# Kernel tuning notes

Measured on AMD Instinct MI355X. Metric: run time of the kernel, lower is better.

The kernel has to match this reference:

```python
import jax, jax.numpy as jnp
import numpy as np

BIG_K = 13
EPS = 1e-5  # torch BatchNorm2d default


def setup_inputs() -> dict:
    key = jax.random.key(0)
    k1, k2, k3, k4 = jax.random.split(key, 4)
    B, C1, C2, H, W_ = 8, 256, 256, 64, 64
    x = jax.random.normal(k1, (B, C1, H, W_), dtype=jnp.float32)
    # scale kernel by fan-in so pre-BN activations are O(1)
    fan_in = C1 * BIG_K * BIG_K
    W = jax.random.normal(k2, (C2, C1, BIG_K, BIG_K), dtype=jnp.float32) / np.sqrt(fan_in)
    gamma = jnp.ones((C2,), dtype=jnp.float32)
    beta = jnp.zeros((C2,), dtype=jnp.float32)
    running_mean = jax.random.normal(k3, (C2,), dtype=jnp.float32) * 0.1
    running_var = jax.random.uniform(k4, (C2,), dtype=jnp.float32, minval=0.5, maxval=1.5)
    return {"x": x, "W": W, "gamma": gamma, "beta": beta,
            "running_mean": running_mean, "running_var": running_var}


def reference(x, W, gamma, beta, running_mean, running_var):
    # Fallback path of ShiftWiseConv: big-kernel conv (no bias) -> BN (inference) -> SiLU
    pad = BIG_K // 2
    y = jax.lax.conv_general_dilated(
        x, W,
        window_strides=(1, 1),
        padding=[(pad, pad), (pad, pad)],
        dimension_numbers=("NCHW", "OIHW", "NCHW"),
    )
    inv = gamma * jax.lax.rsqrt(running_var + EPS)  # [C2]
    y = y * inv[None, :, None, None] + (beta - running_mean * inv)[None, :, None, None]
    return jax.nn.silu(y)
```

## Files before the change

### kernel.cpp

```cpp
#include <hip/hip_runtime.h>
#include <stdint.h>

#define EPS 1e-5f

typedef __attribute__((ext_vector_type(8))) __bf16 bf16x8;
typedef __attribute__((ext_vector_type(16))) float f32x16;

__device__ __forceinline__ int swz4(int r) { return (r ^ (r >> 2)) & 3; }

__device__ __forceinline__ unsigned short f2bf(float f) {
  union { float f; unsigned u; } v; v.f = f;
  unsigned r = v.u + 0x7fffu + ((v.u >> 16) & 1u);
  return (unsigned short)(r >> 16);
}

__device__ __forceinline__ void glds16(const unsigned short* g, unsigned short* l) {
  __builtin_amdgcn_global_load_lds(
      (const __attribute__((address_space(1))) void*)g,
      (__attribute__((address_space(3))) void*)l, 16, 0, 0);
}
__device__ __forceinline__ void glds4(const unsigned short* g, unsigned short* l) {
  __builtin_amdgcn_global_load_lds(
      (const __attribute__((address_space(1))) void*)g,
      (__attribute__((address_space(3))) void*)l, 4, 0, 0);
}

template <int N>
__device__ __forceinline__ void vmwait() {
  asm volatile("s_waitcnt vmcnt(%0)" ::"n"(N) : "memory");
}

__global__ __launch_bounds__(256) void pack_w_kernel(
    const float* __restrict__ W, unsigned short* __restrict__ Wp) {
  const int blk = blockIdx.x;
  const int c2 = blk / 13, kh = blk - c2 * 13;
  const int c1 = threadIdx.x;
  const int c2t = c2 >> 7, m = c2 & 127;
  const int c1c = c1 >> 5, c1i = c1 & 31;
  const float* src = W + (((size_t)(c2 * 256 + c1)) * 13 + kh) * 13;
  const int rowoff = (((c1i >> 3) ^ swz4(m)) << 3) + (c1i & 7);
#pragma unroll
  for (int kw = 0; kw < 13; ++kw) {
    const int ks = (kh * 8 + c1c) * 13 + kw;
    const size_t dst = (((size_t)c2t * 1352 + ks) * 128 + m) * 32 + rowoff;
    Wp[dst] = f2bf(src[kw]);
  }
}

__global__ __launch_bounds__(256) void pack_xt_kernel(
    const float* __restrict__ x, unsigned short* __restrict__ xT) {
  const int blk = blockIdx.x;
  const int rowp = blk % 76;
  const int bc = blk / 76;
  const int c1c = bc & 7, b = bc >> 3;
  const int row = rowp - 6;
  const bool rok = (unsigned)row < 64u;
  unsigned short* dst = xT + (size_t)blk * 2560;
  const float* srcb = x + (size_t)(b * 256 + c1c * 32) * 4096 +
                      (rok ? row * 64 : 0);
#pragma unroll
  for (int e = 0; e < 10; ++e) {
    const int idx = e * 256 + threadIdx.x;
    const int colp = idx >> 5, c1i = idx & 31;
    const int ic = colp - 8;
    const float v = (rok && (unsigned)ic < 64u) ? srcb[(size_t)c1i * 4096 + ic] : 0.f;
    dst[colp * 32 + ((((c1i >> 3) ^ swz4(colp)) << 3)) + (c1i & 7)] = f2bf(v);
  }
}

__global__ __launch_bounds__(256, 2) void conv11_kernel(
    const unsigned short* __restrict__ Wp, const unsigned short* __restrict__ xT,
    const float* __restrict__ gamma, const float* __restrict__ beta,
    const float* __restrict__ mean, const float* __restrict__ var,
    float* __restrict__ out) {
  __shared__ __align__(16) unsigned short Abuf[3][8192];
  __shared__ __align__(16) unsigned short Wbuf[2][5120];
  __shared__ float s_scale[128], s_shift[128];

  const int tid = threadIdx.x;
  const int bid = blockIdx.x;
  const int b = bid & 7;
  const int h0 = ((bid >> 3) & 31) * 2;
  const int c2t = bid >> 8;

  const int wid = tid >> 6, lane = tid & 63;
  const int wr = wid >> 1, wc = wid & 1;
  const int l31 = lane & 31, hi2 = lane >> 5;

  if (tid < 128) {
    const int c2 = c2t * 128 + tid;
    const float inv = gamma[c2] * rsqrtf(var[c2] + EPS);
    s_scale[tid] = inv;
    s_shift[tid] = beta[c2] - mean[c2] * inv;
  }

  int aoffs[2][2];
#pragma unroll
  for (int mt = 0; mt < 2; ++mt)
#pragma unroll
    for (int ks = 0; ks < 2; ++ks) {
      const int m = wr * 64 + mt * 32 + l31;
      aoffs[mt][ks] = m * 64 + (((ks * 2 + hi2) ^ swz4(m)) << 4);
    }
  int ndh[2], nwl[2];
#pragma unroll
  for (int nt = 0; nt < 2; ++nt) {
    const int n = wc * 64 + nt * 32 + l31;
    ndh[nt] = n >> 6;
    nwl[nt] = n & 63;
  }

  const int tid8 = tid * 8, tid2 = tid * 2;
  const int widA = wid * 512, wid128 = wid * 128;

  const size_t c2base = (size_t)c2t * 1352;
  const int bc8 = b * 8;
  const char* Abase = (const char*)&Abuf[0][0];
  unsigned short* AbaseU = &Abuf[0][0];

  auto wtile = [&](int T) -> const unsigned short* {
    const int kh = T >> 3, c1c = T & 7;
    return xT + (size_t)((bc8 + c1c) * 76 + h0 + kh) * 2560;
  };

  f32x16 acc[2][2];
#pragma unroll
  for (int i = 0; i < 2; ++i)
#pragma unroll
    for (int j = 0; j < 2; ++j)
#pragma unroll
      for (int r = 0; r < 16; ++r) acc[i][j][r] = 0.f;

  bf16x8 rE_A[2][2][2], rE_B[2][2][2], rO_A[2][2][2], rO_B[2][2][2];

  int aCur = 0, aNext = 16384, aNN = 32768;

  {
    const unsigned short* ws = wtile(0);
    glds16(ws + tid8, &Wbuf[0][0] + widA);
    glds16(ws + 2048 + tid8, &Wbuf[0][2048] + widA);
    glds4(ws + 4096 + tid2, &Wbuf[0][4096] + wid128);
    glds4(ws + 4608 + tid2, &Wbuf[0][4608] + wid128);
#pragma unroll
    for (int ph = 0; ph < 3; ++ph) {
      const unsigned short* at0 = Wp + ((c2base + 2 * ph) << 12);
      const unsigned short* at1 = Wp + ((c2base + 2 * ph + 1) << 12);
      unsigned short* ad = AbaseU + ph * 8192;
      glds16(at0 + tid8, ad + widA);
      glds16(at0 + 2048 + tid8, ad + 2048 + widA);
      glds16(at1 + tid8, ad + 4096 + widA);
      glds16(at1 + 2048 + tid8, ad + 6144 + widA);
    }
    vmwait<0>();
    __builtin_amdgcn_s_barrier();
    const char* abA = Abase;
    const char* abB = Abase + 8192;
    const char* wb0 = (const char*)&Wbuf[0][0];
#pragma unroll
    for (int ks = 0; ks < 2; ++ks) {
      rE_A[0][ks][0] = *(const bf16x8*)(abA + aoffs[0][ks]);
      rE_A[0][ks][1] = *(const bf16x8*)(abA + aoffs[1][ks]);
      rE_A[1][ks][0] = *(const bf16x8*)(abB + aoffs[0][ks]);
      rE_A[1][ks][1] = *(const bf16x8*)(abB + aoffs[1][ks]);
#pragma unroll
      for (int nt = 0; nt < 2; ++nt) {
        const int cA = nwl[nt] + 0 + 2;
        rE_B[0][ks][nt] = *(const bf16x8*)(wb0 + (ndh[nt] * 80 + cA) * 64 +
                                           (((ks * 2 + hi2) ^ swz4(cA)) << 4));
        const int cB = nwl[nt] + 1 + 2;
        rE_B[1][ks][nt] = *(const bf16x8*)(wb0 + (ndh[nt] * 80 + cB) * 64 +
                                           (((ks * 2 + hi2) ^ swz4(cB)) << 4));
      }
    }
    asm volatile("s_waitcnt lgkmcnt(0)" ::: "memory");
    __builtin_amdgcn_s_barrier();
    __builtin_amdgcn_sched_barrier(0);
  }

#define PHASE(PH, RCA, RCB, RNA, RNB, NKWA, NWBA, NKWB, NWBB, WRT, WSRCP, WDB)\
  {                                                                           \
    __builtin_amdgcn_s_setprio(1);                                            \
                 \
    {                                                                         \
      const char* abA = Abase + aNext;                                        \
      const char* abB = abA + 8192;                                           \
      const char* wbA = (const char*)&Wbuf[(NWBA)][0];                        \
      const char* wbB = (const char*)&Wbuf[(NWBB)][0];                        \
      _Pragma("unroll") for (int ks = 0; ks < 2; ++ks) {                      \
        RNA[0][ks][0] = *(const bf16x8*)(abA + aoffs[0][ks]);                 \
        RNA[0][ks][1] = *(const bf16x8*)(abA + aoffs[1][ks]);                 \
        RNA[1][ks][0] = *(const bf16x8*)(abB + aoffs[0][ks]);                 \
        RNA[1][ks][1] = *(const bf16x8*)(abB + aoffs[1][ks]);                 \
        _Pragma("unroll") for (int nt = 0; nt < 2; ++nt) {                    \
          const int cA = nwl[nt] + (NKWA) + 2;                                \
          RNB[0][ks][nt] = *(const bf16x8*)(                                  \
              wbA + (ndh[nt] * 80 + cA) * 64 +                                \
              (((ks * 2 + hi2) ^ swz4(cA)) << 4));                            \
          const int cB = nwl[nt] + (NKWB) + 2;                                \
          RNB[1][ks][nt] = *(const bf16x8*)(                                  \
              wbB + (ndh[nt] * 80 + cB) * 64 +                                \
              (((ks * 2 + hi2) ^ swz4(cB)) << 4));                            \
        }                                                                     \
      }                                                                       \
    }                                                                         \
             \
    _Pragma("unroll") for (int s = 0; s < 2; ++s)                             \
        _Pragma("unroll") for (int ks = 0; ks < 2; ++ks) {                    \
      acc[0][0] = __builtin_amdgcn_mfma_f32_32x32x16_bf16(                    \
          RCA[s][ks][0], RCB[s][ks][0], acc[0][0], 0, 0, 0);                  \
      acc[0][1] = __builtin_amdgcn_mfma_f32_32x32x16_bf16(                    \
          RCA[s][ks][0], RCB[s][ks][1], acc[0][1], 0, 0, 0);                  \
      acc[1][0] = __builtin_amdgcn_mfma_f32_32x32x16_bf16(                    \
          RCA[s][ks][1], RCB[s][ks][0], acc[1][0], 0, 0, 0);                  \
      acc[1][1] = __builtin_amdgcn_mfma_f32_32x32x16_bf16(                    \
          RCA[s][ks][1], RCB[s][ks][1], acc[1][1], 0, 0, 0);                  \
    }                                                                         \
    __builtin_amdgcn_s_setprio(0);                                            \
    asm volatile("s_waitcnt lgkmcnt(0)" ::: "memory");   \
                                               \
    if ((WRT) == 1) glds16((WSRCP) + tid8, &Wbuf[(WDB)][0] + widA);           \
    if ((WRT) == 2)                                                           \
      glds16((WSRCP) + 2048 + tid8, &Wbuf[(WDB)][2048] + widA);               \
    if ((WRT) == 3) {                                                         \
      glds4((WSRCP) + 4096 + tid2, &Wbuf[(WDB)][4096] + wid128);              \
      glds4((WSRCP) + 4608 + tid2, &Wbuf[(WDB)][4608] + wid128);              \
    }                                                                         \
      \
    {                                                                         \
      int sn0 = S0 + 2 * (PH) + 6;                                            \
      if (sn0 >= 1352) sn0 -= 1352;                                           \
      int sn1 = sn0 + 1;                                                      \
      if (sn1 >= 1352) sn1 -= 1352;                                           \
      const unsigned short* at0 = Wp + ((c2base + (size_t)sn0) << 12);        \
      const unsigned short* at1 = Wp + ((c2base + (size_t)sn1) << 12);        \
      unsigned short* ad = AbaseU + (aCur >> 1);                              \
      glds16(at0 + tid8, ad + widA);                                          \
      glds16(at0 + 2048 + tid8, ad + 2048 + widA);                            \
      glds16(at1 + tid8, ad + 4096 + widA);                                   \
      glds16(at1 + 2048 + tid8, ad + 6144 + widA);                            \
    }                                                                         \
    vmwait<((WRT) == 0 ? 4 : ((WRT) == 3 ? 6 : 5))>();                        \
    __builtin_amdgcn_s_barrier();                                             \
    __builtin_amdgcn_sched_barrier(0);                                        \
    { const int t_ = aCur; aCur = aNext; aNext = aNN; aNN = t_; }             \
  }

  for (int u = 0; u < 26; ++u) {
    const int S0 = u * 52;
    const int Tb = u * 4;
    const unsigned short* wt1 = wtile(Tb + 1);
    const unsigned short* wt2 = wtile(Tb + 2);
    const unsigned short* wt3 = wtile(Tb + 3);
    const unsigned short* wt4 = wtile((Tb + 4 == 104) ? 0 : Tb + 4);
    PHASE(0, rE_A, rE_B, rO_A, rO_B, 2, 0, 3, 0, 0, wt1, 1)
    PHASE(1, rO_A, rO_B, rE_A, rE_B, 4, 0, 5, 0, 1, wt1, 1)
    PHASE(2, rE_A, rE_B, rO_A, rO_B, 6, 0, 7, 0, 2, wt1, 1)
    PHASE(3, rO_A, rO_B, rE_A, rE_B, 8, 0, 9, 0, 3, wt1, 1)
    PHASE(4, rE_A, rE_B, rO_A, rO_B, 10, 0, 11, 0, 0, wt1, 1)
    PHASE(5, rO_A, rO_B, rE_A, rE_B, 12, 0, 0, 1, 0, wt1, 1)
    PHASE(6, rE_A, rE_B, rO_A, rO_B, 1, 1, 2, 1, 0, wt1, 1)
    PHASE(7, rO_A, rO_B, rE_A, rE_B, 3, 1, 4, 1, 1, wt2, 0)
    PHASE(8, rE_A, rE_B, rO_A, rO_B, 5, 1, 6, 1, 2, wt2, 0)
    PHASE(9, rO_A, rO_B, rE_A, rE_B, 7, 1, 8, 1, 3, wt2, 0)
    PHASE(10, rE_A, rE_B, rO_A, rO_B, 9, 1, 10, 1, 0, wt2, 0)
    PHASE(11, rO_A, rO_B, rE_A, rE_B, 11, 1, 12, 1, 0, wt2, 0)
    PHASE(12, rE_A, rE_B, rO_A, rO_B, 0, 0, 1, 0, 0, wt2, 0)
    PHASE(13, rO_A, rO_B, rE_A, rE_B, 2, 0, 3, 0, 0, wt3, 1)
    PHASE(14, rE_A, rE_B, rO_A, rO_B, 4, 0, 5, 0, 1, wt3, 1)
    PHASE(15, rO_A, rO_B, rE_A, rE_B, 6, 0, 7, 0, 2, wt3, 1)
    PHASE(16, rE_A, rE_B, rO_A, rO_B, 8, 0, 9, 0, 3, wt3, 1)
    PHASE(17, rO_A, rO_B, rE_A, rE_B, 10, 0, 11, 0, 0, wt3, 1)
    PHASE(18, rE_A, rE_B, rO_A, rO_B, 12, 0, 0, 1, 0, wt3, 1)
    PHASE(19, rO_A, rO_B, rE_A, rE_B, 1, 1, 2, 1, 0, wt3, 1)
    PHASE(20, rE_A, rE_B, rO_A, rO_B, 3, 1, 4, 1, 1, wt4, 0)
    PHASE(21, rO_A, rO_B, rE_A, rE_B, 5, 1, 6, 1, 2, wt4, 0)
    PHASE(22, rE_A, rE_B, rO_A, rO_B, 7, 1, 8, 1, 3, wt4, 0)
    PHASE(23, rO_A, rO_B, rE_A, rE_B, 9, 1, 10, 1, 0, wt4, 0)
    PHASE(24, rE_A, rE_B, rO_A, rO_B, 11, 1, 12, 1, 0, wt4, 0)
    PHASE(25, rO_A, rO_B, rE_A, rE_B, 0, 0, 1, 0, 0, wt4, 0)
  }
#undef PHASE

  vmwait<0>();

#pragma unroll
  for (int mt = 0; mt < 2; ++mt) {
#pragma unroll
    for (int nt = 0; nt < 2; ++nt) {
      const int n = wc * 64 + nt * 32 + l31;
      const int hh = h0 + (n >> 6), ww = n & 63;
#pragma unroll
      for (int r = 0; r < 16; ++r) {
        const int mloc = (r & 3) + 8 * (r >> 2) + 4 * hi2;
        const int c2l = wr * 64 + mt * 32 + mloc;
        const float y = acc[mt][nt][r] * s_scale[c2l] + s_shift[c2l];
        out[((size_t)(b * 256 + c2t * 128 + c2l)) * 4096 + hh * 64 + ww] =
            y / (1.f + __expf(-y));
      }
    }
  }
}

__global__ void naive_conv_kernel(
    const float* __restrict__ x, const float* __restrict__ W,
    const float* __restrict__ gamma, const float* __restrict__ beta,
    const float* __restrict__ mean, const float* __restrict__ var,
    float* __restrict__ out) {
  const int idx = blockIdx.x * 256 + threadIdx.x;
  if (idx >= 8 * 256 * 64 * 64) return;
  const int w = idx & 63, h = (idx >> 6) & 63;
  const int c2 = (idx >> 12) & 255, b = idx >> 20;
  float s = 0.f;
  for (int c1 = 0; c1 < 256; ++c1) {
    const float* xp = x + ((size_t)(b * 256 + c1) * 4096);
    const float* wp = W + ((size_t)(c2 * 256 + c1) * 169);
    for (int kh = 0; kh < 13; ++kh) {
      const int r = h + kh - 6;
      if ((unsigned)r >= 64u) continue;
      for (int kw = 0; kw < 13; ++kw) {
        const int c = w + kw - 6;
        if ((unsigned)c >= 64u) continue;
        s += xp[r * 64 + c] * wp[kh * 13 + kw];
      }
    }
  }
  const float inv = gamma[c2] * rsqrtf(var[c2] + EPS);
  const float y = s * inv + (beta[c2] - mean[c2] * inv);
  out[idx] = y / (1.f + __expf(-y));
}

extern "C" void kernel_launch(void* const* d_in, const int* in_sizes, int n_in,
                              void* d_out, int out_size, void* d_ws, size_t ws_size,
                              hipStream_t stream) {
  const float* x = (const float*)d_in[0];
  const float* W = (const float*)d_in[1];
  const float* gamma = (const float*)d_in[2];
  const float* beta = (const float*)d_in[3];
  const float* mean = (const float*)d_in[4];
  const float* var = (const float*)d_in[5];
  float* out = (float*)d_out;

  const size_t WP_BYTES = (size_t)256 * 43264 * 2;
  const size_t XT_BYTES = (size_t)12455424 * 2;

  if (ws_size >= WP_BYTES + XT_BYTES) {
    unsigned short* Wp = (unsigned short*)d_ws;
    unsigned short* xT = (unsigned short*)((char*)d_ws + WP_BYTES);
    pack_w_kernel<<<256 * 13, 256, 0, stream>>>(W, Wp);
    pack_xt_kernel<<<8 * 8 * 76, 256, 0, stream>>>(x, xT);
    conv11_kernel<<<512, 256, 0, stream>>>(Wp, xT, gamma, beta, mean, var, out);
  } else {
    naive_conv_kernel<<<(8 * 256 * 64 * 64 + 255) / 256, 256, 0, stream>>>(
        x, W, gamma, beta, mean, var, out);
  }
}
```

Before: 607.9 us.

## Add split-K conv kernel with larger 512-thread tiles and separate reduce+BN+SiLU pass

Adds a new conv kernel that splits the reduction dimension into two halves across blocks. Each 512-thread block computes a 128x256 output tile covering four rows, using double-buffered weight and input LDS staging with loads issued before the MFMAs. The fp32 partial sums go to a workspace buffer, and a new vectorized kernel adds the two halves and applies BN and SiLU. The larger tiles are meant to improve data reuse and the split-K to add parallelism. In exchange it costs an extra 64MB write and read of partials plus one more launch, and it needs a larger workspace, falling back to the old path otherwise.

New measurement: 1.572 ms. 2.59x slower.

```diff
diff --git a/kernel.cpp b/kernel.cpp
--- a/kernel.cpp
+++ b/kernel.cpp
@@ -5,6 +5,7 @@
 
 typedef __attribute__((ext_vector_type(8))) __bf16 bf16x8;
 typedef __attribute__((ext_vector_type(16))) float f32x16;
+typedef __attribute__((ext_vector_type(4))) float f32x4;
 
 __device__ __forceinline__ int swz4(int r) { return (r ^ (r >> 2)) & 3; }
 
@@ -68,6 +69,253 @@
   }
 }
 
+__global__ __launch_bounds__(512, 4) void conv14_kernel(
+    const unsigned short* __restrict__ Wp, const unsigned short* __restrict__ xT,
+    float* __restrict__ Ppart) {
+  __shared__ __align__(16) unsigned short Abuf[2][8192];
+  __shared__ __align__(16) unsigned short Wbuf[2][10240];
+
+  const int tid = threadIdx.x;
+  const int bid = blockIdx.x;
+  const int b = bid & 7;
+  const int hq = (bid >> 3) & 15;
+  const int c2t = (bid >> 7) & 1;
+  const int kHalf = bid >> 8;
+  const int h0 = hq * 4;
+
+  const int wid = tid >> 6, lane = tid & 63;
+  const int wr = wid >> 2, wn = wid & 3;
+  const int l31 = lane & 31, hi2 = lane >> 5;
+
+  int aoffs[2][2];
+#pragma unroll
+  for (int mt = 0; mt < 2; ++mt)
+#pragma unroll
+    for (int ks = 0; ks < 2; ++ks) {
+      const int m = wr * 64 + mt * 32 + l31;
+      aoffs[mt][ks] = m * 64 + (((ks * 2 + hi2) ^ swz4(m)) << 4);
+    }
+  int ndh[2], nwl[2];
+#pragma unroll
+  for (int nt = 0; nt < 2; ++nt) {
+    const int n = wn * 64 + nt * 32 + l31;
+    ndh[nt] = n >> 6;
+    nwl[nt] = n & 63;
+  }
+
+  const int tid8 = tid * 8, tid2 = tid * 2;
+  const int widA = wid * 512;
+  const int wid128 = wid * 128;
+
+  const size_t c2base = (size_t)c2t * 1352;
+  const int kBaseStep = kHalf * 676;
+  const int kBaseTile = kHalf * 52;
+  const int bc8 = b * 8;
+  const char* Abase = (const char*)&Abuf[0][0];
+  unsigned short* AbaseU = &Abuf[0][0];
+
+  auto wtile = [&](int Tloc) -> const unsigned short* {
+    const int T = kBaseTile + Tloc;
+    const int kh = T >> 3, c1c = T & 7;
+    return xT + (size_t)((bc8 + c1c) * 76 + h0 + kh) * 2560;
+  };
+
+  f32x16 acc[2][2];
+#pragma unroll
+  for (int i = 0; i < 2; ++i)
+#pragma unroll
+    for (int j = 0; j < 2; ++j)
+#pragma unroll
+      for (int r = 0; r < 16; ++r) acc[i][j][r] = 0.f;
+
+  bf16x8 rE_A[2][2][2], rE_B[2][2][2], rO_A[2][2][2], rO_B[2][2][2];
+
+  int aWr = 0, aRd = 16384;
+
+  {
+    const unsigned short* ws = wtile(0);
+    glds16(ws + tid8, &Wbuf[0][0] + widA);
+    glds16(ws + 4096 + tid8, &Wbuf[0][4096] + widA);
+    glds4(ws + 8192 + tid2, &Wbuf[0][8192] + wid128);
+    glds4(ws + 9216 + tid2, &Wbuf[0][9216] + wid128);
+#pragma unroll
+    for (int s = 0; s < 4; ++s) {
+      const unsigned short* at =
+          Wp + ((c2base + (size_t)(kBaseStep + s)) << 12);
+      glds16(at + tid8, AbaseU + s * 4096 + widA);
+    }
+    vmwait<0>();
+    __builtin_amdgcn_s_barrier();
+    const char* abA = Abase;
+    const char* abB = Abase + 8192;
+    const char* wb0 = (const char*)&Wbuf[0][0];
+#pragma unroll
+    for (int ks = 0; ks < 2; ++ks) {
+      rE_A[0][ks][0] = *(const bf16x8*)(abA + aoffs[0][ks]);
+      rE_A[0][ks][1] = *(const bf16x8*)(abA + aoffs[1][ks]);
+      rE_A[1][ks][0] = *(const bf16x8*)(abB + aoffs[0][ks]);
+      rE_A[1][ks][1] = *(const bf16x8*)(abB + aoffs[1][ks]);
+#pragma unroll
+      for (int nt = 0; nt < 2; ++nt) {
+        const int cA = nwl[nt] + 0 + 2;
+        rE_B[0][ks][nt] = *(const bf16x8*)(wb0 + (ndh[nt] * 80 + cA) * 64 +
+                                           (((ks * 2 + hi2) ^ swz4(cA)) << 4));
+        const int cB = nwl[nt] + 1 + 2;
+        rE_B[1][ks][nt] = *(const bf16x8*)(wb0 + (ndh[nt] * 80 + cB) * 64 +
+                                           (((ks * 2 + hi2) ^ swz4(cB)) << 4));
+      }
+    }
+    asm volatile("s_waitcnt lgkmcnt(0)" ::: "memory");
+    __builtin_amdgcn_s_barrier();
+    __builtin_amdgcn_sched_barrier(0);
+  }
+
+#define PHASE(PH, RCA, RCB, RNA, RNB, NKWA, NWBA, NKWB, NWBB, WRT, WSRCP,     \
+              WDPAR)                                                          \
+  {                                                                           \
+    {                \
+      int sl0 = S0 + 2 * (PH) + 4;                                            \
+      if (sl0 >= 676) sl0 -= 676;                                             \
+      int sl1 = sl0 + 1;                                                      \
+      if (sl1 >= 676) sl1 -= 676;                                             \
+      const unsigned short* at0 =                                             \
+          Wp + ((c2base + (size_t)(kBaseStep + sl0)) << 12);                  \
+      const unsigned short* at1 =                                             \
+          Wp + ((c2base + (size_t)(kBaseStep + sl1)) << 12);                  \
+      unsigned short* ad = AbaseU + (aWr >> 1);                               \
+      glds16(at0 + tid8, ad + widA);                                          \
+      glds16(at1 + tid8, ad + 4096 + widA);                                   \
+    }                                                                         \
+    if ((WRT) == 1) glds16((WSRCP) + tid8, &Wbuf[(WDPAR)][0] + widA);         \
+    if ((WRT) == 2)                                                           \
+      glds16((WSRCP) + 4096 + tid8, &Wbuf[(WDPAR)][4096] + widA);             \
+    if ((WRT) == 3) {                                                         \
+      glds4((WSRCP) + 8192 + tid2, &Wbuf[(WDPAR)][8192] + wid128);            \
+      glds4((WSRCP) + 9216 + tid2, &Wbuf[(WDPAR)][9216] + wid128);            \
+    }                                                                         \
+    __builtin_amdgcn_s_setprio(1);                                            \
+    {                                            \
+      const char* abA = Abase + aRd;                                          \
+      const char* abB = abA + 8192;                                           \
+      const char* wbA = (const char*)&Wbuf[(NWBA)][0];                        \
+      const char* wbB = (const char*)&Wbuf[(NWBB)][0];                        \
+      _Pragma("unroll") for (int ks = 0; ks < 2; ++ks) {                      \
+        RNA[0][ks][0] = *(const bf16x8*)(abA + aoffs[0][ks]);                 \
+        RNA[0][ks][1] = *(const bf16x8*)(abA + aoffs[1][ks]);                 \
+        RNA[1][ks][0] = *(const bf16x8*)(abB + aoffs[0][ks]);                 \
+        RNA[1][ks][1] = *(const bf16x8*)(abB + aoffs[1][ks]);                 \
+        _Pragma("unroll") for (int nt = 0; nt < 2; ++nt) {                    \
+          const int cA = nwl[nt] + (NKWA) + 2;                                \
+          RNB[0][ks][nt] = *(const bf16x8*)(                                  \
+              wbA + (ndh[nt] * 80 + cA) * 64 +                                \
+              (((ks * 2 + hi2) ^ swz4(cA)) << 4));                            \
+          const int cB = nwl[nt] + (NKWB) + 2;                                \
+          RNB[1][ks][nt] = *(const bf16x8*)(                                  \
+              wbB + (ndh[nt] * 80 + cB) * 64 +                                \
+              (((ks * 2 + hi2) ^ swz4(cB)) << 4));                            \
+        }                                                                     \
+      }                                                                       \
+    }                                                                         \
+                                                \
+    _Pragma("unroll") for (int s = 0; s < 2; ++s)                             \
+        _Pragma("unroll") for (int ks = 0; ks < 2; ++ks) {                    \
+      acc[0][0] = __builtin_amdgcn_mfma_f32_32x32x16_bf16(                    \
+          RCA[s][ks][0], RCB[s][ks][0], acc[0][0], 0, 0, 0);                  \
+      acc[0][1] = __builtin_amdgcn_mfma_f32_32x32x16_bf16(                    \
+          RCA[s][ks][0], RCB[s][ks][1], acc[0][1], 0, 0, 0);                  \
+      acc[1][0] = __builtin_amdgcn_mfma_f32_32x32x16_bf16(                    \
+          RCA[s][ks][1], RCB[s][ks][0], acc[1][0], 0, 0, 0);                  \
+      acc[1][1] = __builtin_amdgcn_mfma_f32_32x32x16_bf16(                    \
+          RCA[s][ks][1], RCB[s][ks][1], acc[1][1], 0, 0, 0);                  \
+    }                                                                         \
+    __builtin_amdgcn_s_setprio(0);                                            \
+    asm volatile("s_waitcnt lgkmcnt(0)" ::: "memory");                        \
+    vmwait<((WRT) == 0 ? 0 : ((WRT) == 3 ? 2 : 1))>();                        \
+    __builtin_amdgcn_s_barrier();                                             \
+    __builtin_amdgcn_sched_barrier(0);                                        \
+    { const int t_ = aWr; aWr = aRd; aRd = t_; }                              \
+  }
+
+  for (int u = 0; u < 13; ++u) {
+    const int S0 = u * 52;
+    const int Tb = u * 4;
+    const unsigned short* wt1 = wtile((Tb + 1) % 52);
+    const unsigned short* wt2 = wtile((Tb + 2) % 52);
+    const unsigned short* wt3 = wtile((Tb + 3) % 52);
+    const unsigned short* wt4 = wtile((Tb + 4) % 52);
+    PHASE(0, rE_A, rE_B, rO_A, rO_B, 2, 0, 3, 0, 1, wt1, 1)
+    PHASE(1, rO_A, rO_B, rE_A, rE_B, 4, 0, 5, 0, 2, wt1, 1)
+    PHASE(2, rE_A, rE_B, rO_A, rO_B, 6, 0, 7, 0, 3, wt1, 1)
+    PHASE(3, rO_A, rO_B, rE_A, rE_B, 8, 0, 9, 0, 0, wt1, 1)
+    PHASE(4, rE_A, rE_B, rO_A, rO_B, 10, 0, 11, 0, 0, wt1, 1)
+    PHASE(5, rO_A, rO_B, rE_A, rE_B, 12, 0, 0, 1, 0, wt1, 1)
+    PHASE(6, rE_A, rE_B, rO_A, rO_B, 1, 1, 2, 1, 0, wt1, 1)
+    PHASE(7, rO_A, rO_B, rE_A, rE_B, 3, 1, 4, 1, 1, wt2, 0)
+    PHASE(8, rE_A, rE_B, rO_A, rO_B, 5, 1, 6, 1, 2, wt2, 0)
+    PHASE(9, rO_A, rO_B, rE_A, rE_B, 7, 1, 8, 1, 3, wt2, 0)
+    PHASE(10, rE_A, rE_B, rO_A, rO_B, 9, 1, 10, 1, 0, wt2, 0)
+    PHASE(11, rO_A, rO_B, rE_A, rE_B, 11, 1, 12, 1, 0, wt2, 0)
+    PHASE(12, rE_A, rE_B, rO_A, rO_B, 0, 0, 1, 0, 0, wt2, 0)
+    PHASE(13, rO_A, rO_B, rE_A, rE_B, 2, 0, 3, 0, 1, wt3, 1)
+    PHASE(14, rE_A, rE_B, rO_A, rO_B, 4, 0, 5, 0, 2, wt3, 1)
+    PHASE(15, rO_A, rO_B, rE_A, rE_B, 6, 0, 7, 0, 3, wt3, 1)
+    PHASE(16, rE_A, rE_B, rO_A, rO_B, 8, 0, 9, 0, 0, wt3, 1)
+    PHASE(17, rO_A, rO_B, rE_A, rE_B, 10, 0, 11, 0, 0, wt3, 1)
+    PHASE(18, rE_A, rE_B, rO_A, rO_B, 12, 0, 0, 1, 0, wt3, 1)
+    PHASE(19, rO_A, rO_B, rE_A, rE_B, 1, 1, 2, 1, 0, wt3, 1)
+    PHASE(20, rE_A, rE_B, rO_A, rO_B, 3, 1, 4, 1, 1, wt4, 0)
+    PHASE(21, rO_A, rO_B, rE_A, rE_B, 5, 1, 6, 1, 2, wt4, 0)
+    PHASE(22, rE_A, rE_B, rO_A, rO_B, 7, 1, 8, 1, 3, wt4, 0)
+    PHASE(23, rO_A, rO_B, rE_A, rE_B, 9, 1, 10, 1, 0, wt4, 0)
+    PHASE(24, rE_A, rE_B, rO_A, rO_B, 11, 1, 12, 1, 0, wt4, 0)
+    PHASE(25, rO_A, rO_B, rE_A, rE_B, 0, 0, 1, 0, 0, wt4, 0)
+  }
+#undef PHASE
+
+  vmwait<0>();
+
+#pragma unroll
+  for (int mt = 0; mt < 2; ++mt) {
+#pragma unroll
+    for (int nt = 0; nt < 2; ++nt) {
+      const int n = wn * 64 + nt * 32 + l31;
+      const int hh = h0 + (n >> 6), ww = n & 63;
+#pragma unroll
+      for (int r = 0; r < 16; ++r) {
+        const int mloc = (r & 3) + 8 * (r >> 2) + 4 * hi2;
+        const int c2l = wr * 64 + mt * 32 + mloc;
+        Ppart[(size_t)kHalf * 8388608 +
+              ((size_t)(b * 256 + c2t * 128 + c2l)) * 4096 + hh * 64 + ww] =
+            acc[mt][nt][r];
+      }
+    }
+  }
+}
+
+__global__ __launch_bounds__(256) void reduce_bn_silu_kernel(
+    const float* __restrict__ Ppart, const float* __restrict__ gamma,
+    const float* __restrict__ beta, const float* __restrict__ mean,
+    const float* __restrict__ var, float* __restrict__ out) {
+  const int i = blockIdx.x * 256 + threadIdx.x;
+  const f32x4* p0 = (const f32x4*)Ppart;
+  const f32x4* p1 = (const f32x4*)(Ppart + 8388608);
+  f32x4* o4 = (f32x4*)out;
+#pragma unroll
+  for (int rr = 0; rr < 4; ++rr) {
+    const int i4 = i + rr * 524288;
+    f32x4 v = p0[i4] + p1[i4];
+    const int c2 = (i4 >> 10) & 255;
+    const float inv = gamma[c2] * rsqrtf(var[c2] + EPS);
+    const float sh = beta[c2] - mean[c2] * inv;
+#pragma unroll
+    for (int j = 0; j < 4; ++j) {
+      const float y = v[j] * inv + sh;
+      v[j] = y / (1.f + __expf(-y));
+    }
+    o4[i4] = v;
+  }
+}
+
 __global__ __launch_bounds__(256, 2) void conv11_kernel(
     const unsigned short* __restrict__ Wp, const unsigned short* __restrict__ xT,
     const float* __restrict__ gamma, const float* __restrict__ beta,
@@ -132,7 +380,6 @@
       for (int r = 0; r < 16; ++r) acc[i][j][r] = 0.f;
 
   bf16x8 rE_A[2][2][2], rE_B[2][2][2], rO_A[2][2][2], rO_B[2][2][2];
-
   int aCur = 0, aNext = 16384, aNN = 32768;
 
   {
@@ -180,7 +427,6 @@
 #define PHASE(PH, RCA, RCB, RNA, RNB, NKWA, NWBA, NKWB, NWBB, WRT, WSRCP, WDB)\
   {                                                                           \
     __builtin_amdgcn_s_setprio(1);                                            \
-                 \
     {                                                                         \
       const char* abA = Abase + aNext;                                        \
       const char* abB = abA + 8192;                                           \
@@ -203,7 +449,6 @@
         }                                                                     \
       }                                                                       \
     }                                                                         \
-             \
     _Pragma("unroll") for (int s = 0; s < 2; ++s)                             \
         _Pragma("unroll") for (int ks = 0; ks < 2; ++ks) {                    \
       acc[0][0] = __builtin_amdgcn_mfma_f32_32x32x16_bf16(                    \
@@ -216,8 +461,7 @@
           RCA[s][ks][1], RCB[s][ks][1], acc[1][1], 0, 0, 0);                  \
     }                                                                         \
     __builtin_amdgcn_s_setprio(0);                                            \
-    asm volatile("s_waitcnt lgkmcnt(0)" ::: "memory");   \
-                                               \
+    asm volatile("s_waitcnt lgkmcnt(0)" ::: "memory");                        \
     if ((WRT) == 1) glds16((WSRCP) + tid8, &Wbuf[(WDB)][0] + widA);           \
     if ((WRT) == 2)                                                           \
       glds16((WSRCP) + 2048 + tid8, &Wbuf[(WDB)][2048] + widA);               \
@@ -225,7 +469,6 @@
       glds4((WSRCP) + 4096 + tid2, &Wbuf[(WDB)][4096] + wid128);              \
       glds4((WSRCP) + 4608 + tid2, &Wbuf[(WDB)][4608] + wid128);              \
     }                                                                         \
-      \
     {                                                                         \
       int sn0 = S0 + 2 * (PH) + 6;                                            \
       if (sn0 >= 1352) sn0 -= 1352;                                           \
@@ -342,8 +585,18 @@
 
   const size_t WP_BYTES = (size_t)256 * 43264 * 2;
   const size_t XT_BYTES = (size_t)12455424 * 2;
-
-  if (ws_size >= WP_BYTES + XT_BYTES) {
+  const size_t P_BYTES = (size_t)2 * 8388608 * 4;
+
+  if (ws_size >= WP_BYTES + XT_BYTES + P_BYTES) {
+    unsigned short* Wp = (unsigned short*)d_ws;
+    unsigned short* xT = (unsigned short*)((char*)d_ws + WP_BYTES);
+    float* Ppart = (float*)((char*)d_ws + WP_BYTES + XT_BYTES);
+    pack_w_kernel<<<256 * 13, 256, 0, stream>>>(W, Wp);
+    pack_xt_kernel<<<8 * 8 * 76, 256, 0, stream>>>(x, xT);
+    conv14_kernel<<<512, 512, 0, stream>>>(Wp, xT, Ppart);
+    reduce_bn_silu_kernel<<<2048, 256, 0, stream>>>(Ppart, gamma, beta, mean,
+                                                    var, out);
+  } else if (ws_size >= WP_BYTES + XT_BYTES) {
     unsigned short* Wp = (unsigned short*)d_ws;
     unsigned short* xT = (unsigned short*)((char*)d_ws + WP_BYTES);
     pack_w_kernel<<<256 * 13, 256, 0, stream>>>(W, Wp);
```
